# Kernel tuning notes

Measured on AMD Instinct MI355X. Metric: run time of the kernel, lower is better.

## Reference

```python
import jax, jax.numpy as jnp
import numpy as np

B, NS, NQ = 128, 128, 512
D_IN, D_OUT = 256, 64


def setup_inputs() -> dict:
    key = jax.random.key(0)
    ks = jax.random.split(key, 6)
    return {
        "phi_support": jax.random.normal(ks[0], (B, NS, D_IN), dtype=jnp.float32),
        "y_support": jax.random.normal(ks[1], (B, NS, D_OUT), dtype=jnp.float32),
        "phi_query": jax.random.normal(ks[2], (B, NQ, D_IN), dtype=jnp.float32),
        "y_query": jax.random.normal(ks[3], (B, NQ, D_OUT), dtype=jnp.float32),
        # xavier-uniform-ish params
        "m_prior": jax.random.uniform(ks[4], (D_IN, D_OUT), minval=-1.0, maxval=1.0) * np.sqrt(6.0 / (D_IN + D_OUT)),
        "S_inv_prior_asym": jax.random.uniform(ks[5], (D_IN, D_IN), minval=-1.0, maxval=1.0) * np.sqrt(6.0 / (2 * D_IN)),
        "sig_eps": jnp.array([0.1], dtype=jnp.float32),
    }


def reference(phi_support, y_support, phi_query, y_query, m_prior, S_inv_prior_asym, sig_eps):
    alpha = 1.0
    d_out = m_prior.shape[1]
    # prior precision (symmetric PSD by construction) and natural-param prior mean
    S_inv_prior = alpha * (S_inv_prior_asym @ S_inv_prior_asym.T)          # [D_in, D_in]
    m_prior_nat = S_inv_prior @ m_prior                                     # [D_in, D_out]
    # posterior precision / covariance per task (nobs > 0 branch)
    S_inv = jnp.einsum('bni,bnj->bij', phi_support, phi_support) + S_inv_prior  # [B, D_in, D_in]
    S = jnp.linalg.inv(S_inv)                                               # batched small inverse
    rhs = jnp.einsum('bni,bnk->bik', phi_support, y_support) + m_prior_nat  # [B, D_in, D_out]
    m = S @ rhs                                                             # [B, D_in, D_out]
    # predictive mean and spread
    mu = phi_query @ m                                                      # [B, Q, D_out]
    spread_fac = 1.0 + jnp.einsum('bqi,bij,bqj->bq', phi_query, S, phi_query)  # [B, Q]
    # sig = spread_fac (x) (eye * sig_eps) : diagonal [B, Q, D_out, D_out]
    diag = jnp.eye(d_out, dtype=mu.dtype) * sig_eps                         # [D_out, D_out]
    sig = spread_fac[..., None, None] * diag
    # nll: logdet of diagonal sig + quadratic form with its inverse (diag -> reciprocal)
    logdet = d_out * (jnp.log(spread_fac) + jnp.log(sig_eps))               # [B, Q]
    resid = y_query - mu
    quadf = jnp.sum(resid * resid, axis=-1) / (spread_fac * sig_eps)        # [B, Q]
    nll = logdet.mean() + quadf.mean()
    return mu, sig, nll
```

## Files before the change

### kernel.cpp

```cpp
#include <hip/hip_runtime.h>
#include <math.h>

#define B_T   128
#define NS    128
#define NQ    512
#define DIN   256
#define DOUT  64

#define MU_SIZE  (B_T*NQ*DOUT)
#define SIG_SIZE (B_T*NQ*DOUT*DOUT)
#define NLL_IDX  (MU_SIZE + SIG_SIZE)

__global__ __launch_bounds__(256) void k_prior_sp(const float* __restrict__ A,
                                                  double* __restrict__ Sp,
                                                  double* __restrict__ NLLACC) {
    __shared__ float Ai[16][260];
    __shared__ float Aj[16][260];
    int bi = blockIdx.x;
    int i0 = (bi >> 4) << 4;
    int j0 = (bi & 15) << 4;
    int tid = threadIdx.x;
    if (bi == 0 && tid == 0) NLLACC[0] = 0.0;
    for (int idx = tid; idx < 16 * 256; idx += 256) {
        int r = idx >> 8, c = idx & 255;
        Ai[r][c] = A[(i0 + r) * 256 + c];
        Aj[r][c] = A[(j0 + r) * 256 + c];
    }
    __syncthreads();
    int r = tid >> 4, c = tid & 15;
    double acc = 0.0;
    for (int k = 0; k < 256; ++k)
        acc += (double)Ai[r][k] * (double)Aj[c][k];
    Sp[(i0 + r) * 256 + (j0 + c)] = acc;
}

__global__ __launch_bounds__(64) void k_prior_mpn(const double* __restrict__ Sp,
                                                  const float* __restrict__ MP,
                                                  double* __restrict__ MPN) {
    int i = blockIdx.x, k = threadIdx.x;
    double acc = 0.0;
    for (int t = 0; t < 256; ++t)
        acc += Sp[i * 256 + t] * (double)MP[t * 64 + k];
    MPN[i * 64 + k] = acc;
}

__global__ __launch_bounds__(256) void k_build_G(const float* __restrict__ PHI,
                                                 const double* __restrict__ Sp,
                                                 double* __restrict__ G) {
    __shared__ float As[128][64];
    __shared__ float Bs[128][64];
    int b = blockIdx.x;
    int by = blockIdx.y;
    int ti = 0;
    while (((ti + 1) * (ti + 2)) / 2 <= by) ti++;
    int tj = by - (ti * (ti + 1)) / 2;
    int i0 = ti * 64, j0 = tj * 64;
    int tid = threadIdx.x;
    const float* Pb = PHI + b * (NS * DIN);
    for (int idx = tid; idx < 128 * 64; idx += 256) {
        int n = idx >> 6, c = idx & 63;
        As[n][c] = Pb[n * 256 + i0 + c];
        Bs[n][c] = Pb[n * 256 + j0 + c];
    }
    __syncthreads();
    int tx = tid & 15, ty = tid >> 4;
    double acc[4][4];
#pragma unroll
    for (int r = 0; r < 4; ++r)
#pragma unroll
        for (int s = 0; s < 4; ++s) acc[r][s] = 0.0;
    for (int n = 0; n < 128; ++n) {
        float a0 = As[n][4 * ty + 0], a1 = As[n][4 * ty + 1];
        float a2 = As[n][4 * ty + 2], a3 = As[n][4 * ty + 3];
        float b0 = Bs[n][4 * tx + 0], b1 = Bs[n][4 * tx + 1];
        float b2 = Bs[n][4 * tx + 2], b3 = Bs[n][4 * tx + 3];
        acc[0][0] += (double)a0 * b0; acc[0][1] += (double)a0 * b1;
        acc[0][2] += (double)a0 * b2; acc[0][3] += (double)a0 * b3;
        acc[1][0] += (double)a1 * b0; acc[1][1] += (double)a1 * b1;
        acc[1][2] += (double)a1 * b2; acc[1][3] += (double)a1 * b3;
        acc[2][0] += (double)a2 * b0; acc[2][1] += (double)a2 * b1;
        acc[2][2] += (double)a2 * b2; acc[2][3] += (double)a2 * b3;
        acc[3][0] += (double)a3 * b0; acc[3][1] += (double)a3 * b1;
        acc[3][2] += (double)a3 * b2; acc[3][3] += (double)a3 * b3;
    }
    double* Gb = G + b * 65536;
#pragma unroll
    for (int r = 0; r < 4; ++r) {
        int i = i0 + 4 * ty + r;
#pragma unroll
        for (int s = 0; s < 4; ++s) {
            int j = j0 + 4 * tx + s;
            Gb[i * 256 + j] = acc[r][s] + Sp[i * 256 + j];
        }
    }
}

__global__ __launch_bounds__(256) void k_build_rhs(const float* __restrict__ PHI,
                                                   const float* __restrict__ Y,
                                                   const double* __restrict__ MPN,
                                                   double* __restrict__ RHS) {
    __shared__ float As[128][64];
    __shared__ float Ys[128][64];
    int b = blockIdx.x, i0 = blockIdx.y * 64, tid = threadIdx.x;
    const float* Pb = PHI + b * (NS * DIN);
    const float* Yb = Y + b * (NS * DOUT);
    for (int idx = tid; idx < 128 * 64; idx += 256) {
        int n = idx >> 6, c = idx & 63;
        As[n][c] = Pb[n * 256 + i0 + c];
        Ys[n][c] = Yb[n * 64 + c];
    }
    __syncthreads();
    int tx = tid & 15, ty = tid >> 4;
    double acc[4][4];
#pragma unroll
    for (int r = 0; r < 4; ++r)
#pragma unroll
        for (int s = 0; s < 4; ++s) acc[r][s] = 0.0;
    for (int n = 0; n < 128; ++n) {
        float a0 = As[n][4 * ty + 0], a1 = As[n][4 * ty + 1];
        float a2 = As[n][4 * ty + 2], a3 = As[n][4 * ty + 3];
        float y0 = Ys[n][4 * tx + 0], y1 = Ys[n][4 * tx + 1];
        float y2 = Ys[n][4 * tx + 2], y3 = Ys[n][4 * tx + 3];
        acc[0][0] += (double)a0 * y0; acc[0][1] += (double)a0 * y1;
        acc[0][2] += (double)a0 * y2; acc[0][3] += (double)a0 * y3;
        acc[1][0] += (double)a1 * y0; acc[1][1] += (double)a1 * y1;
        acc[1][2] += (double)a1 * y2; acc[1][3] += (double)a1 * y3;
        acc[2][0] += (double)a2 * y0; acc[2][1] += (double)a2 * y1;
        acc[2][2] += (double)a2 * y2; acc[2][3] += (double)a2 * y3;
        acc[3][0] += (double)a3 * y0; acc[3][1] += (double)a3 * y1;
        acc[3][2] += (double)a3 * y2; acc[3][3] += (double)a3 * y3;
    }
    double* Rb = RHS + b * 16384;
#pragma unroll
    for (int r = 0; r < 4; ++r) {
        int i = i0 + 4 * ty + r;
#pragma unroll
        for (int s = 0; s < 4; ++s) {
            int kc = 4 * tx + s;
            Rb[i * 64 + kc] = acc[r][s] + MPN[i * 64 + kc];
        }
    }
}

__global__ __launch_bounds__(256) void k_potrf64(const double* __restrict__ G,
                                                 double* __restrict__ LT,
                                                 double* __restrict__ LI,
                                                 int kb) {
    __shared__ double D[64][65];
    __shared__ double T[64][33];
    __shared__ double C[32][33];
    __shared__ double L11s[16 * 17];
    __shared__ double DINVs[16];
    int b = blockIdx.x, tid = threadIdx.x;
    int o = kb * 64;
    const double* Gb = G + b * 65536;
    double* LTb = LT + b * 65536;
    double* LIb = LI + b * 16384 + kb * 4096;
    for (int idx = tid; idx < 4096; idx += 256) {
        int r = idx >> 6, c = idx & 63;
        D[r][c] = Gb[(o + r) * 256 + o + c];
    }
    __syncthreads();
    for (int p0 = 0; p0 < 64; p0 += 16) {
        if (tid < 64) {
            int lane = tid;
            double a[16];
            if (lane < 16) {
#pragma unroll
                for (int p = 0; p < 16; ++p) a[p] = D[p0 + lane][p0 + p];
            }
#pragma unroll
            for (int p = 0; p < 16; ++p) {
                double dp = __shfl(a[p], p);
                double d = sqrt(fmax(dp, 1e-300));
                double inv = 1.0 / d;
                if (lane == p) { a[p] = d; DINVs[p] = inv; }
                else if (lane > p) a[p] *= inv;
#pragma unroll
                for (int p2 = p + 1; p2 < 16; ++p2) {
                    double cc = __shfl(a[p], p2);
                    if (lane > p) a[p2] -= a[p] * cc;
                }
            }
            if (lane < 16) {
#pragma unroll
                for (int p = 0; p < 16; ++p) {
                    if (p <= lane) {
                        L11s[lane * 17 + p] = a[p];
                        D[p0 + lane][p0 + p] = a[p];
                    }
                }
            }
        }
        __syncthreads();
        int nsolve = 48 - p0;
        if (tid < nsolve) {
            int rr = p0 + 16 + tid;
            double x[16];
#pragma unroll
            for (int p = 0; p < 16; ++p) {
                double s = D[rr][p0 + p];
#pragma unroll
                for (int p2 = 0; p2 < 16; ++p2) {
                    if (p2 < p) s -= L11s[p * 17 + p2] * x[p2];
                }
                x[p] = s * DINVs[p];
                D[rr][p0 + p] = x[p];
            }
        }
        __syncthreads();
        int rem = nsolve;
        for (int idx = tid; idx < rem * rem; idx += 256) {
            int i2 = idx / rem, j2 = idx - i2 * rem;
            if (j2 <= i2) {
                int i = p0 + 16 + i2, j = p0 + 16 + j2;
                double s = 0.0;
#pragma unroll
                for (int p = 0; p < 16; ++p) s += D[i][p0 + p] * D[j][p0 + p];
                D[i][j] -= s;
            }
        }
        __syncthreads();
    }
    for (int idx = tid; idx < 4096; idx += 256) {
        int c = idx >> 6, r = idx & 63;
        if (r >= c) LTb[(o + c) * 256 + (o + r)] = D[r][c];
    }
    if (tid < 64) {
        int g = tid >> 5, j = tid & 31;
        int off = g * 32;
        double x[32];
#pragma unroll
        for (int i = 0; i < 32; ++i) {
            double s = (i == j) ? 1.0 : 0.0;
#pragma unroll
            for (int k = 0; k < i; ++k) {
                double lv = D[off + i][off + k];
                s -= (k >= j) ? lv * x[k] : 0.0;
            }
            double inv = 1.0 / D[off + i][off + i];
            x[i] = (i >= j) ? s * inv : 0.0;
        }
#pragma unroll
        for (int i = 0; i < 32; ++i) T[off + i][j] = x[i];
    }
    __syncthreads();
    for (int idx = tid; idx < 1024; idx += 256) {
        int r = idx >> 5, c = idx & 31;
        double s = 0.0;
#pragma unroll
        for (int p = 0; p < 32; ++p) s += D[32 + r][p] * T[p][c];
        C[r][c] = s;
    }
    __syncthreads();
    for (int idx = tid; idx < 1024; idx += 256) {
        int r = idx >> 5, c = idx & 31;
        double s = 0.0;
#pragma unroll
        for (int p = 0; p < 32; ++p) s += T[32 + r][p] * C[p][c];
        D[32 + r][c] = -s;
    }
    __syncthreads();
    for (int idx = tid; idx < 4096; idx += 256) {
        int p = idx >> 6, c = idx & 63;
        double v;
        if (c < 32) v = (p < 32) ? T[c][p] : 0.0;
        else        v = (p < 32) ? D[c][p] : T[c][p - 32];
        LIb[p * 64 + c] = v;
    }
}

__global__ __launch_bounds__(256) void k_trsm64(const double* __restrict__ G,
                                                const double* __restrict__ LI,
                                                double* __restrict__ LT,
                                                int kb) {
    __shared__ double Gs[64][65];
    __shared__ double Ls[64][65];
    int b = blockIdx.x;
    int i0 = (kb + 1 + blockIdx.y) * 64;
    int o = kb * 64;
    int tid = threadIdx.x;
    const double* Gb = G + b * 65536;
    const double* LIb = LI + b * 16384 + kb * 4096;
    double* LTb = LT + b * 65536;
    for (int idx = tid; idx < 4096; idx += 256) {
        int r = idx >> 6, c = idx & 63;
        Gs[r][c] = Gb[(i0 + r) * 256 + o + c];
        Ls[r][c] = LIb[idx];
    }
    __syncthreads();
    int tx = tid & 15, ty = tid >> 4;
    double acc[4][4];
#pragma unroll
    for (int r = 0; r < 4; ++r)
#pragma unroll
        for (int s = 0; s < 4; ++s) acc[r][s] = 0.0;
    for (int kk = 0; kk < 64; ++kk) {
        double a0 = Gs[4 * ty + 0][kk], a1 = Gs[4 * ty + 1][kk];
        double a2 = Gs[4 * ty + 2][kk], a3 = Gs[4 * ty + 3][kk];
        double b0 = Ls[kk][4 * tx + 0], b1 = Ls[kk][4 * tx + 1];
        double b2 = Ls[kk][4 * tx + 2], b3 = Ls[kk][4 * tx + 3];
        acc[0][0] += a0 * b0; acc[0][1] += a0 * b1; acc[0][2] += a0 * b2; acc[0][3] += a0 * b3;
        acc[1][0] += a1 * b0; acc[1][1] += a1 * b1; acc[1][2] += a1 * b2; acc[1][3] += a1 * b3;
        acc[2][0] += a2 * b0; acc[2][1] += a2 * b1; acc[2][2] += a2 * b2; acc[2][3] += a2 * b3;
        acc[3][0] += a3 * b0; acc[3][1] += a3 * b1; acc[3][2] += a3 * b2; acc[3][3] += a3 * b3;
    }
#pragma unroll
    for (int r = 0; r < 4; ++r)
#pragma unroll
        for (int s = 0; s < 4; ++s)
            LTb[(o + 4 * tx + s) * 256 + i0 + 4 * ty + r] = acc[r][s];
}

__global__ __launch_bounds__(256) void k_syrk64(const double* __restrict__ LT,
                                                double* __restrict__ G,
                                                int kb) {
    __shared__ double LiT[64][65];
    __shared__ double LjT[64][65];
    int b = blockIdx.x, py = blockIdx.y;
    int ti = 0;
    while (((ti + 1) * (ti + 2)) / 2 <= py) ti++;
    int tj = py - (ti * (ti + 1)) / 2;
    int i0 = (kb + 1 + ti) * 64, j0 = (kb + 1 + tj) * 64;
    int o = kb * 64;
    int tid = threadIdx.x;
    const double* LTb = LT + b * 65536;
    double* Gb = G + b * 65536;
    for (int idx = tid; idx < 4096; idx += 256) {
        int p = idx >> 6, r = idx & 63;
        LiT[p][r] = LTb[(o + p) * 256 + i0 + r];
        LjT[p][r] = LTb[(o + p) * 256 + j0 + r];
    }
    __syncthreads();
    int tx = tid & 15, ty = tid >> 4;
    double acc[4][4];
#pragma unroll
    for (int r = 0; r < 4; ++r)
#pragma unroll
        for (int s = 0; s < 4; ++s) acc[r][s] = 0.0;
    for (int kk = 0; kk < 64; ++kk) {
        double a0 = LiT[kk][4 * ty + 0], a1 = LiT[kk][4 * ty + 1];
        double a2 = LiT[kk][4 * ty + 2], a3 = LiT[kk][4 * ty + 3];
        double b0 = LjT[kk][4 * tx + 0], b1 = LjT[kk][4 * tx + 1];
        double b2 = LjT[kk][4 * tx + 2], b3 = LjT[kk][4 * tx + 3];
        acc[0][0] += a0 * b0; acc[0][1] += a0 * b1; acc[0][2] += a0 * b2; acc[0][3] += a0 * b3;
        acc[1][0] += a1 * b0; acc[1][1] += a1 * b1; acc[1][2] += a1 * b2; acc[1][3] += a1 * b3;
        acc[2][0] += a2 * b0; acc[2][1] += a2 * b1; acc[2][2] += a2 * b2; acc[2][3] += a2 * b3;
        acc[3][0] += a3 * b0; acc[3][1] += a3 * b1; acc[3][2] += a3 * b2; acc[3][3] += a3 * b3;
    }
#pragma unroll
    for (int r = 0; r < 4; ++r) {
        int gi = i0 + 4 * ty + r;
#pragma unroll
        for (int s = 0; s < 4; ++s) {
            int gj = j0 + 4 * tx + s;
            Gb[gi * 256 + gj] -= acc[r][s];
        }
    }
}

__global__ __launch_bounds__(256) void k_diaginv(const double* __restrict__ LT,
                                                 double* __restrict__ TI,
                                                 float* __restrict__ TIF) {
    __shared__ double SHD[8192];
    int b = blockIdx.x, tid = threadIdx.x;
    const double* LTb = LT + b * 65536;
    double* TIb = TI + b * 65536;
    float* TIFb = TIF + b * 65536;
    for (int idx = tid; idx < 65536; idx += 256) {
        int i = idx >> 8, k = idx & 255;
        if (k > i) { TIb[idx] = 0.0; TIFb[idx] = 0.0f; }
    }
    for (int idx = tid; idx < 8192; idx += 256) {
        int g = idx >> 10, rem = idx & 1023, k = rem >> 5, i = rem & 31;
        SHD[idx] = LTb[(32 * g + k) * 256 + 32 * g + i];
    }
    __syncthreads();
    int g = tid >> 5, j = tid & 31;
    const double* D = SHD + g * 1024;
    double x[32];
#pragma unroll
    for (int i = 0; i < 32; ++i) {
        double s = (i == j) ? 1.0 : 0.0;
#pragma unroll
        for (int k = 0; k < i; ++k) {
            double lv = D[k * 32 + i];
            s -= (k >= j) ? lv * x[k] : 0.0;
        }
        double inv = 1.0 / D[i * 32 + i];
        x[i] = (i >= j) ? s * inv : 0.0;
    }
#pragma unroll
    for (int i = 0; i < 32; ++i) {
        int gi = 32 * g + i, gj = 32 * g + j;
        TIb[gi * 256 + gj] = x[i];
        TIFb[gi * 256 + gj] = (float)x[i];
    }
}

__global__ __launch_bounds__(256) void k_trinv(const double* __restrict__ LT,
                                               double* __restrict__ TI,
                                               float* __restrict__ TIF) {
    __shared__ double XS[8][1024];
    int b = blockIdx.x, J = blockIdx.y;
    int tid = threadIdx.x, j = tid & 31, ig = tid >> 5;
    const double* LTb = LT + b * 65536;
    double* TIb = TI + b * 65536;
    float* TIFb = TIF + b * 65536;
    double* Bsh = XS[7];

    for (int idx = tid; idx < 1024; idx += 256) {
        int kk = idx >> 5, c = idx & 31;
        XS[J][idx] = TIb[(32 * J + kk) * 256 + 32 * J + c];
    }
    __syncthreads();

    for (int I = J + 1; I < 8; ++I) {
        double acc[4] = {0.0, 0.0, 0.0, 0.0};
        for (int K = J; K < I; ++K) {
            for (int idx = tid; idx < 1024; idx += 256) {
                int kk = idx >> 5, i2 = idx & 31;
                Bsh[idx] = LTb[(32 * K + kk) * 256 + 32 * I + i2];
            }
            __syncthreads();
            const double* Xk = XS[K];
            for (int kk = 0; kk < 32; ++kk) {
                double tv = Xk[kk * 32 + j];
#pragma unroll
                for (int r = 0; r < 4; ++r)
                    acc[r] += Bsh[kk * 32 + ig * 4 + r] * tv;
            }
            __syncthreads();
        }
#pragma unroll
        for (int r = 0; r < 4; ++r) Bsh[(ig * 4 + r) * 32 + j] = acc[r];
        __syncthreads();
        double c[4] = {0.0, 0.0, 0.0, 0.0};
        for (int k = 0; k < 32; ++k) {
            double bv = Bsh[k * 32 + j];
#pragma unroll
            for (int r = 0; r < 4; ++r)
                c[r] -= TIb[(32 * I + ig * 4 + r) * 256 + 32 * I + k] * bv;
        }
#pragma unroll
        for (int r = 0; r < 4; ++r) {
            int gi = 32 * I + ig * 4 + r, gj = 32 * J + j;
            TIb[gi * 256 + gj] = c[r];
            TIFb[gi * 256 + gj] = (float)c[r];
            if (I < 7) XS[I][(ig * 4 + r) * 32 + j] = c[r];
        }
        __syncthreads();
    }
}

__global__ __launch_bounds__(256) void k_gemm_Z(const double* __restrict__ TI,
                                                const double* __restrict__ RHS,
                                                double* __restrict__ Z) {
    __shared__ double As[32][64];
    __shared__ double Bs[64][64];
    int b = blockIdx.x, i0 = blockIdx.y * 32;
    int tid = threadIdx.x, c = tid & 63, rg = tid >> 6;
    const double* TIb = TI + b * 65536;
    const double* Rb = RHS + b * 16384;
    double* Zb = Z + b * 16384;
    double acc[8] = {};
    for (int k0 = 0; k0 <= i0; k0 += 64) {
        for (int idx = tid; idx < 2048; idx += 256) {
            int r = idx >> 6, kk = idx & 63;
            As[r][kk] = TIb[(i0 + r) * 256 + k0 + kk];
        }
        for (int idx = tid; idx < 4096; idx += 256) {
            int kk = idx >> 6, cc = idx & 63;
            Bs[kk][cc] = Rb[(k0 + kk) * 64 + cc];
        }
        __syncthreads();
        for (int kk = 0; kk < 64; ++kk) {
            double bv = Bs[kk][c];
#pragma unroll
            for (int r = 0; r < 8; ++r)
                acc[r] += As[rg * 8 + r][kk] * bv;
        }
        __syncthreads();
    }
#pragma unroll
    for (int r = 0; r < 8; ++r)
        Zb[(i0 + rg * 8 + r) * 64 + c] = acc[r];
}

__global__ __launch_bounds__(256) void k_gemm_M(const double* __restrict__ TI,
                                                const double* __restrict__ Z,
                                                double* __restrict__ M) {
    __shared__ double As[64][32];
    __shared__ double Bs[64][64];
    int b = blockIdx.x, i0 = blockIdx.y * 32;
    int tid = threadIdx.x, c = tid & 63, rg = tid >> 6;
    const double* TIb = TI + b * 65536;
    const double* Zb = Z + b * 16384;
    double* Mb = M + b * 16384;
    double acc[8] = {};
    for (int k0 = (i0 >> 6) << 6; k0 < 256; k0 += 64) {
        for (int idx = tid; idx < 2048; idx += 256) {
            int kk = idx >> 5, ri = idx & 31;
            As[kk][ri] = TIb[(k0 + kk) * 256 + i0 + ri];
        }
        for (int idx = tid; idx < 4096; idx += 256) {
            int kk = idx >> 6, cc = idx & 63;
            Bs[kk][cc] = Zb[(k0 + kk) * 64 + cc];
        }
        __syncthreads();
        for (int kk = 0; kk < 64; ++kk) {
            double bv = Bs[kk][c];
#pragma unroll
            for (int r = 0; r < 8; ++r)
                acc[r] += As[kk][rg * 8 + r] * bv;
        }
        __syncthreads();
    }
#pragma unroll
    for (int r = 0; r < 8; ++r)
        Mb[(i0 + rg * 8 + r) * 64 + c] = acc[r];
}

__global__ __launch_bounds__(256) void k_spread_gemm(const float* __restrict__ PHIQ,
                                                     const float* __restrict__ TIF,
                                                     float* __restrict__ PSUM) {
    __shared__ float Qs[64][65];
    __shared__ float Ts[64][65];
    int b = blockIdx.x, q0 = blockIdx.y * 64, I = blockIdx.z, i0 = I * 64;
    int tid = threadIdx.x, tx = tid & 15, ty = tid >> 4;
    const float* Qb = PHIQ + b * (NQ * DIN) + q0 * DIN;
    const float* Tb = TIF + b * 65536;
    float acc[4][4];
#pragma unroll
    for (int r = 0; r < 4; ++r)
#pragma unroll
        for (int s = 0; s < 4; ++s) acc[r][s] = 0.0f;
    for (int k0 = 0; k0 <= i0; k0 += 64) {
        for (int idx = tid; idx < 4096; idx += 256) {
            int r = idx >> 6, c = idx & 63;
            Qs[r][c] = Qb[r * 256 + k0 + c];
            Ts[c][r] = Tb[(i0 + r) * 256 + k0 + c];
        }
        __syncthreads();
        for (int kk = 0; kk < 64; ++kk) {
            float a0 = Qs[4 * ty + 0][kk], a1 = Qs[4 * ty + 1][kk];
            float a2 = Qs[4 * ty + 2][kk], a3 = Qs[4 * ty + 3][kk];
            float b0 = Ts[kk][4 * tx + 0], b1 = Ts[kk][4 * tx + 1];
            float b2 = Ts[kk][4 * tx + 2], b3 = Ts[kk][4 * tx + 3];
            acc[0][0] += a0 * b0; acc[0][1] += a0 * b1; acc[0][2] += a0 * b2; acc[0][3] += a0 * b3;
            acc[1][0] += a1 * b0; acc[1][1] += a1 * b1; acc[1][2] += a1 * b2; acc[1][3] += a1 * b3;
            acc[2][0] += a2 * b0; acc[2][1] += a2 * b1; acc[2][2] += a2 * b2; acc[2][3] += a2 * b3;
            acc[3][0] += a3 * b0; acc[3][1] += a3 * b1; acc[3][2] += a3 * b2; acc[3][3] += a3 * b3;
        }
        __syncthreads();
    }
#pragma unroll
    for (int r = 0; r < 4; ++r) {
        float p = acc[r][0] * acc[r][0] + acc[r][1] * acc[r][1]
                + acc[r][2] * acc[r][2] + acc[r][3] * acc[r][3];
        p += __shfl_down(p, 8, 16);
        p += __shfl_down(p, 4, 16);
        p += __shfl_down(p, 2, 16);
        p += __shfl_down(p, 1, 16);
        if (tx == 0) PSUM[(size_t)(b * 4 + I) * 512 + q0 + 4 * ty + r] = p;
    }
}

__global__ __launch_bounds__(256) void k_mu_nll(const float* __restrict__ PHIQ,
                                                const double* __restrict__ M,
                                                const float* __restrict__ YQ,
                                                const float* __restrict__ PSUM,
                                                const float* __restrict__ SE,
                                                float* __restrict__ SPREAD,
                                                double* __restrict__ NLLACC,
                                                float* __restrict__ MU) {
    __shared__ float Qs[64][65];
    __shared__ float Ms[64][64];
    __shared__ double nred[64];
    int b = blockIdx.x, q0 = blockIdx.y * 64, tid = threadIdx.x;
    int tx = tid & 15, ty = tid >> 4;
    const float* Qb = PHIQ + b * (NQ * DIN) + q0 * DIN;
    const double* Mb = M + b * 16384;
    float acc[4][4];
#pragma unroll
    for (int r = 0; r < 4; ++r)
#pragma unroll
        for (int s = 0; s < 4; ++s) acc[r][s] = 0.0f;
    for (int c0 = 0; c0 < 256; c0 += 64) {
        for (int idx = tid; idx < 4096; idx += 256) {
            int r = idx >> 6, c = idx & 63;
            Qs[r][c] = Qb[r * 256 + c0 + c];
            Ms[r][c] = (float)Mb[(c0 + r) * 64 + c];
        }
        __syncthreads();
        for (int kk = 0; kk < 64; ++kk) {
            float a0 = Qs[4 * ty + 0][kk], a1 = Qs[4 * ty + 1][kk];
            float a2 = Qs[4 * ty + 2][kk], a3 = Qs[4 * ty + 3][kk];
            float b0 = Ms[kk][4 * tx + 0], b1 = Ms[kk][4 * tx + 1];
            float b2 = Ms[kk][4 * tx + 2], b3 = Ms[kk][4 * tx + 3];
            acc[0][0] += a0 * b0; acc[0][1] += a0 * b1; acc[0][2] += a0 * b2; acc[0][3] += a0 * b3;
            acc[1][0] += a1 * b0; acc[1][1] += a1 * b1; acc[1][2] += a1 * b2; acc[1][3] += a1 * b3;
            acc[2][0] += a2 * b0; acc[2][1] += a2 * b1; acc[2][2] += a2 * b2; acc[2][3] += a2 * b3;
            acc[3][0] += a3 * b0; acc[3][1] += a3 * b1; acc[3][2] += a3 * b2; acc[3][3] += a3 * b3;
        }
        __syncthreads();
    }
    float se = SE[0];
#pragma unroll
    for (int r = 0; r < 4; ++r) {
        int q = q0 + 4 * ty + r;
        float4 v = make_float4(acc[r][0], acc[r][1], acc[r][2], acc[r][3]);
        *(float4*)&MU[(b * NQ + q) * 64 + 4 * tx] = v;
        float4 y = *(const float4*)&YQ[(size_t)(b * NQ + q) * 64 + 4 * tx];
        float dx = y.x - v.x, dy = y.y - v.y, dz = y.z - v.z, dw = y.w - v.w;
        float qs = dx * dx + dy * dy + dz * dz + dw * dw;
        qs += __shfl_down(qs, 8, 16);
        qs += __shfl_down(qs, 4, 16);
        qs += __shfl_down(qs, 2, 16);
        qs += __shfl_down(qs, 1, 16);
        if (tx == 0) {
            float sp = 1.0f + PSUM[(size_t)(b * 4 + 0) * 512 + q]
                            + PSUM[(size_t)(b * 4 + 1) * 512 + q]
                            + PSUM[(size_t)(b * 4 + 2) * 512 + q]
                            + PSUM[(size_t)(b * 4 + 3) * 512 + q];
            SPREAD[b * 512 + q] = sp;
            float val = 64.0f * (logf(sp) + logf(se)) + qs / (sp * se);
            nred[ty * 4 + r] = (double)val;
        }
    }
    __syncthreads();
    for (int s = 32; s > 0; s >>= 1) {
        if (tid < s) nred[tid] += nred[tid + s];
        __syncthreads();
    }
    if (tid == 0) atomicAdd(NLLACC, nred[0] * (1.0 / 65536.0));
}

__global__ void k_nll_final(const double* __restrict__ NLLACC,
                            float* __restrict__ out) {
    if (threadIdx.x == 0) out[NLL_IDX] = (float)NLLACC[0];
}

__global__ __launch_bounds__(256) void k_sig(const float* __restrict__ SPREAD,
                                             const float* __restrict__ SE,
                                             float* __restrict__ out) {
    __shared__ float sv_s;
    int bq = blockIdx.x, tid = threadIdx.x;
    if (tid == 0) sv_s = SPREAD[bq] * SE[0];
    __syncthreads();
    float sv = sv_s;
    float* base = out + (size_t)MU_SIZE + (size_t)bq * 4096;
    int i = tid >> 2;
    int jb = (tid & 3) << 4;
    int d = i - jb;
    float vals[16];
#pragma unroll
    for (int t = 0; t < 16; ++t) vals[t] = (t == d) ? sv : 0.0f;
    float4* p = (float4*)(base + tid * 16);
    p[0] = make_float4(vals[0], vals[1], vals[2], vals[3]);
    p[1] = make_float4(vals[4], vals[5], vals[6], vals[7]);
    p[2] = make_float4(vals[8], vals[9], vals[10], vals[11]);
    p[3] = make_float4(vals[12], vals[13], vals[14], vals[15]);
}

extern "C" void kernel_launch(void* const* d_in, const int* in_sizes, int n_in,
                              void* d_out, int out_size, void* d_ws, size_t ws_size,
                              hipStream_t stream) {
    const float* PHI_S = (const float*)d_in[0];
    const float* Y_S   = (const float*)d_in[1];
    const float* PHI_Q = (const float*)d_in[2];
    const float* Y_Q   = (const float*)d_in[3];
    const float* MP    = (const float*)d_in[4];
    const float* AP    = (const float*)d_in[5];
    const float* SE    = (const float*)d_in[6];
    float* out = (float*)d_out;

    double* scratch = (double*)(out + MU_SIZE);
    double* G    = scratch;
    double* LT   = G + 8388608;
    double* RHS  = LT + 8388608;
    double* Z    = RHS + 2097152;
    double* TI   = Z + 2097152;
    double* Spd  = TI + 8388608;
    double* MPN  = Spd + 65536;
    double* LI   = MPN + 16384;
    float*  TIF  = (float*)(LI + 2097152);
    float*  PSUM = TIF + 8388608;
    float*  SPREAD = (float*)d_ws;
    double* NLLACC = (double*)((char*)d_ws + 65536 * 4);

    k_prior_sp   <<<256, 256, 0, stream>>>(AP, Spd, NLLACC);
    k_prior_mpn  <<<256, 64, 0, stream>>>(Spd, MP, MPN);
    k_build_G    <<<dim3(B_T, 10), 256, 0, stream>>>(PHI_S, Spd, G);
    k_build_rhs  <<<dim3(B_T, 4), 256, 0, stream>>>(PHI_S, Y_S, MPN, RHS);
    const int syrk_pairs[3] = {6, 3, 1};
    for (int kb = 0; kb < 4; ++kb) {
        k_potrf64<<<B_T, 256, 0, stream>>>(G, LT, LI, kb);
        if (kb < 3) {
            k_trsm64<<<dim3(B_T, 3 - kb), 256, 0, stream>>>(G, LI, LT, kb);
            k_syrk64<<<dim3(B_T, syrk_pairs[kb]), 256, 0, stream>>>(LT, G, kb);
        }
    }
    k_diaginv    <<<B_T, 256, 0, stream>>>(LT, TI, TIF);
    k_trinv      <<<dim3(B_T, 7), 256, 0, stream>>>(LT, TI, TIF);
    k_gemm_Z     <<<dim3(B_T, 8), 256, 0, stream>>>(TI, RHS, Z);
    k_gemm_M     <<<dim3(B_T, 8), 256, 0, stream>>>(TI, Z, RHS);
    k_spread_gemm<<<dim3(B_T, 8, 4), 256, 0, stream>>>(PHI_Q, TIF, PSUM);
    k_mu_nll     <<<dim3(B_T, 8), 256, 0, stream>>>(PHI_Q, RHS, Y_Q, PSUM, SE,
                                                    SPREAD, NLLACC, out);
    k_nll_final  <<<1, 64, 0, stream>>>(NLLACC, out);
    k_sig        <<<65536, 256, 0, stream>>>(SPREAD, SE, out);
}
```

Before: 2.090 ms.

## Use FP64 MFMA for small batched GEMMs with runtime layout probe

Replaces the scalar FP64 FMA inner loops in build_G, build_rhs, trsm, syrk and the Z/M GEMMs with 16x16x4 FP64 MFMA intrinsics. A one-wave probe kernel runs first, works out the MFMA output lane-to-element mapping, and writes a flag that each kernel reads to choose its store indexing, falling back to the scalar path if no mapping matches. The Z/M GEMMs also move to 64-row tiles, halving their grids. This targets the FP64 compute-bound parts of the Cholesky-based solve, but adds an extra launch, a flag load per block, and branch code. The total is likely dominated by the large sig output write, which is unchanged.

```diff
diff --git a/kernel.cpp b/kernel.cpp
--- a/kernel.cpp
+++ b/kernel.cpp
@@ -10,6 +10,53 @@
 #define MU_SIZE  (B_T*NQ*DOUT)
 #define SIG_SIZE (B_T*NQ*DOUT*DOUT)
 #define NLL_IDX  (MU_SIZE + SIG_SIZE)
+
+typedef double v4df __attribute__((ext_vector_type(4)));
+
+__device__ __forceinline__ void dmap(int fl, int kq, int mrow, int rr,
+                                     int& lr, int& lc) {
+    if (fl == 0)      { lr = kq * 4 + rr; lc = mrow; }
+    else if (fl == 1) { lr = kq + 4 * rr; lc = mrow; }
+    else if (fl == 2) { lr = mrow; lc = kq * 4 + rr; }
+    else              { lr = mrow; lc = kq + 4 * rr; }
+}
+
+__global__ void k_mfma_probe(double* __restrict__ FLAGD) {
+    int l = threadIdx.x;
+    int m = l & 15, q = l >> 4;
+    double a = (double)(1 + m + 2 * q);
+    double b = (double)(1 + 3 * m + 5 * q);
+    v4df d = {0.0, 0.0, 0.0, 0.0};
+    d = __builtin_amdgcn_mfma_f64_16x16x4f64(a, b, d, 0, 0, 0);
+    bool ok0 = true, ok1 = true, ok2 = true, ok3 = true;
+#pragma unroll
+    for (int r = 0; r < 4; ++r) {
+        int rows[4] = {4 * q + r, q + 4 * r, m, m};
+        int cols[4] = {m, m, 4 * q + r, q + 4 * r};
+        double ref[4];
+#pragma unroll
+        for (int v = 0; v < 4; ++v) {
+            double s = 0.0;
+#pragma unroll
+            for (int k = 0; k < 4; ++k)
+                s += (double)(1 + rows[v] + 2 * k) * (double)(1 + 3 * cols[v] + 5 * k);
+            ref[v] = s;
+        }
+        if (d[r] != ref[0]) ok0 = false;
+        if (d[r] != ref[1]) ok1 = false;
+        if (d[r] != ref[2]) ok2 = false;
+        if (d[r] != ref[3]) ok3 = false;
+    }
+    ok0 = __all(ok0); ok1 = __all(ok1); ok2 = __all(ok2); ok3 = __all(ok3);
+    if (l == 0) {
+        double f = 99.0;
+        if (ok0) f = 0.0;
+        else if (ok1) f = 1.0;
+        else if (ok2) f = 2.0;
+        else if (ok3) f = 3.0;
+        FLAGD[0] = f;
+    }
+}
 
 __global__ __launch_bounds__(256) void k_prior_sp(const float* __restrict__ A,
                                                   double* __restrict__ Sp,
@@ -46,7 +93,8 @@
 
 __global__ __launch_bounds__(256) void k_build_G(const float* __restrict__ PHI,
                                                  const double* __restrict__ Sp,
-                                                 double* __restrict__ G) {
+                                                 double* __restrict__ G,
+                                                 const double* __restrict__ FLAGD) {
     __shared__ float As[128][64];
     __shared__ float Bs[128][64];
     int b = blockIdx.x;
@@ -63,34 +111,61 @@
         Bs[n][c] = Pb[n * 256 + j0 + c];
     }
     __syncthreads();
-    int tx = tid & 15, ty = tid >> 4;
-    double acc[4][4];
-#pragma unroll
-    for (int r = 0; r < 4; ++r)
-#pragma unroll
-        for (int s = 0; s < 4; ++s) acc[r][s] = 0.0;
-    for (int n = 0; n < 128; ++n) {
-        float a0 = As[n][4 * ty + 0], a1 = As[n][4 * ty + 1];
-        float a2 = As[n][4 * ty + 2], a3 = As[n][4 * ty + 3];
-        float b0 = Bs[n][4 * tx + 0], b1 = Bs[n][4 * tx + 1];
-        float b2 = Bs[n][4 * tx + 2], b3 = Bs[n][4 * tx + 3];
-        acc[0][0] += (double)a0 * b0; acc[0][1] += (double)a0 * b1;
-        acc[0][2] += (double)a0 * b2; acc[0][3] += (double)a0 * b3;
-        acc[1][0] += (double)a1 * b0; acc[1][1] += (double)a1 * b1;
-        acc[1][2] += (double)a1 * b2; acc[1][3] += (double)a1 * b3;
-        acc[2][0] += (double)a2 * b0; acc[2][1] += (double)a2 * b1;
-        acc[2][2] += (double)a2 * b2; acc[2][3] += (double)a2 * b3;
-        acc[3][0] += (double)a3 * b0; acc[3][1] += (double)a3 * b1;
-        acc[3][2] += (double)a3 * b2; acc[3][3] += (double)a3 * b3;
-    }
     double* Gb = G + b * 65536;
-#pragma unroll
-    for (int r = 0; r < 4; ++r) {
-        int i = i0 + 4 * ty + r;
-#pragma unroll
-        for (int s = 0; s < 4; ++s) {
-            int j = j0 + 4 * tx + s;
-            Gb[i * 256 + j] = acc[r][s] + Sp[i * 256 + j];
+    int fl = (int)FLAGD[0];
+    if (fl < 4) {
+        int lane = tid & 63, w = tid >> 6;
+        int mrow = lane & 15, kq = lane >> 4;
+        v4df acc[4];
+#pragma unroll
+        for (int t = 0; t < 4; ++t) acc[t] = (v4df){0.0, 0.0, 0.0, 0.0};
+        for (int ks = 0; ks < 128; ks += 4) {
+            double a = (double)As[ks + kq][w * 16 + mrow];
+#pragma unroll
+            for (int t = 0; t < 4; ++t) {
+                double bb = (double)Bs[ks + kq][t * 16 + mrow];
+                acc[t] = __builtin_amdgcn_mfma_f64_16x16x4f64(a, bb, acc[t], 0, 0, 0);
+            }
+        }
+#pragma unroll
+        for (int t = 0; t < 4; ++t) {
+#pragma unroll
+            for (int rr = 0; rr < 4; ++rr) {
+                int lr, lc; dmap(fl, kq, mrow, rr, lr, lc);
+                int i = i0 + w * 16 + lr;
+                int j = j0 + t * 16 + lc;
+                Gb[i * 256 + j] = acc[t][rr] + Sp[i * 256 + j];
+            }
+        }
+    } else {
+        int tx = tid & 15, ty = tid >> 4;
+        double acc[4][4];
+#pragma unroll
+        for (int r = 0; r < 4; ++r)
+#pragma unroll
+            for (int s = 0; s < 4; ++s) acc[r][s] = 0.0;
+        for (int n = 0; n < 128; ++n) {
+            float a0 = As[n][4 * ty + 0], a1 = As[n][4 * ty + 1];
+            float a2 = As[n][4 * ty + 2], a3 = As[n][4 * ty + 3];
+            float b0 = Bs[n][4 * tx + 0], b1 = Bs[n][4 * tx + 1];
+            float b2 = Bs[n][4 * tx + 2], b3 = Bs[n][4 * tx + 3];
+            acc[0][0] += (double)a0 * b0; acc[0][1] += (double)a0 * b1;
+            acc[0][2] += (double)a0 * b2; acc[0][3] += (double)a0 * b3;
+            acc[1][0] += (double)a1 * b0; acc[1][1] += (double)a1 * b1;
+            acc[1][2] += (double)a1 * b2; acc[1][3] += (double)a1 * b3;
+            acc[2][0] += (double)a2 * b0; acc[2][1] += (double)a2 * b1;
+            acc[2][2] += (double)a2 * b2; acc[2][3] += (double)a2 * b3;
+            acc[3][0] += (double)a3 * b0; acc[3][1] += (double)a3 * b1;
+            acc[3][2] += (double)a3 * b2; acc[3][3] += (double)a3 * b3;
+        }
+#pragma unroll
+        for (int r = 0; r < 4; ++r) {
+            int i = i0 + 4 * ty + r;
+#pragma unroll
+            for (int s = 0; s < 4; ++s) {
+                int j = j0 + 4 * tx + s;
+                Gb[i * 256 + j] = acc[r][s] + Sp[i * 256 + j];
+            }
         }
     }
 }
@@ -98,7 +173,8 @@
 __global__ __launch_bounds__(256) void k_build_rhs(const float* __restrict__ PHI,
                                                    const float* __restrict__ Y,
                                                    const double* __restrict__ MPN,
-                                                   double* __restrict__ RHS) {
+                                                   double* __restrict__ RHS,
+                                                   const double* __restrict__ FLAGD) {
     __shared__ float As[128][64];
     __shared__ float Ys[128][64];
     int b = blockIdx.x, i0 = blockIdx.y * 64, tid = threadIdx.x;
@@ -110,34 +186,61 @@
         Ys[n][c] = Yb[n * 64 + c];
     }
     __syncthreads();
-    int tx = tid & 15, ty = tid >> 4;
-    double acc[4][4];
-#pragma unroll
-    for (int r = 0; r < 4; ++r)
-#pragma unroll
-        for (int s = 0; s < 4; ++s) acc[r][s] = 0.0;
-    for (int n = 0; n < 128; ++n) {
-        float a0 = As[n][4 * ty + 0], a1 = As[n][4 * ty + 1];
-        float a2 = As[n][4 * ty + 2], a3 = As[n][4 * ty + 3];
-        float y0 = Ys[n][4 * tx + 0], y1 = Ys[n][4 * tx + 1];
-        float y2 = Ys[n][4 * tx + 2], y3 = Ys[n][4 * tx + 3];
-        acc[0][0] += (double)a0 * y0; acc[0][1] += (double)a0 * y1;
-        acc[0][2] += (double)a0 * y2; acc[0][3] += (double)a0 * y3;
-        acc[1][0] += (double)a1 * y0; acc[1][1] += (double)a1 * y1;
-        acc[1][2] += (double)a1 * y2; acc[1][3] += (double)a1 * y3;
-        acc[2][0] += (double)a2 * y0; acc[2][1] += (double)a2 * y1;
-        acc[2][2] += (double)a2 * y2; acc[2][3] += (double)a2 * y3;
-        acc[3][0] += (double)a3 * y0; acc[3][1] += (double)a3 * y1;
-        acc[3][2] += (double)a3 * y2; acc[3][3] += (double)a3 * y3;
-    }
     double* Rb = RHS + b * 16384;
-#pragma unroll
-    for (int r = 0; r < 4; ++r) {
-        int i = i0 + 4 * ty + r;
-#pragma unroll
-        for (int s = 0; s < 4; ++s) {
-            int kc = 4 * tx + s;
-            Rb[i * 64 + kc] = acc[r][s] + MPN[i * 64 + kc];
+    int fl = (int)FLAGD[0];
+    if (fl < 4) {
+        int lane = tid & 63, w = tid >> 6;
+        int mrow = lane & 15, kq = lane >> 4;
+        v4df acc[4];
+#pragma unroll
+        for (int t = 0; t < 4; ++t) acc[t] = (v4df){0.0, 0.0, 0.0, 0.0};
+        for (int ks = 0; ks < 128; ks += 4) {
+            double a = (double)As[ks + kq][w * 16 + mrow];
+#pragma unroll
+            for (int t = 0; t < 4; ++t) {
+                double bb = (double)Ys[ks + kq][t * 16 + mrow];
+                acc[t] = __builtin_amdgcn_mfma_f64_16x16x4f64(a, bb, acc[t], 0, 0, 0);
+            }
+        }
+#pragma unroll
+        for (int t = 0; t < 4; ++t) {
+#pragma unroll
+            for (int rr = 0; rr < 4; ++rr) {
+                int lr, lc; dmap(fl, kq, mrow, rr, lr, lc);
+                int i = i0 + w * 16 + lr;
+                int kc = t * 16 + lc;
+                Rb[i * 64 + kc] = acc[t][rr] + MPN[i * 64 + kc];
+            }
+        }
+    } else {
+        int tx = tid & 15, ty = tid >> 4;
+        double acc[4][4];
+#pragma unroll
+        for (int r = 0; r < 4; ++r)
+#pragma unroll
+            for (int s = 0; s < 4; ++s) acc[r][s] = 0.0;
+        for (int n = 0; n < 128; ++n) {
+            float a0 = As[n][4 * ty + 0], a1 = As[n][4 * ty + 1];
+            float a2 = As[n][4 * ty + 2], a3 = As[n][4 * ty + 3];
+            float y0 = Ys[n][4 * tx + 0], y1 = Ys[n][4 * tx + 1];
+            float y2 = Ys[n][4 * tx + 2], y3 = Ys[n][4 * tx + 3];
+            acc[0][0] += (double)a0 * y0; acc[0][1] += (double)a0 * y1;
+            acc[0][2] += (double)a0 * y2; acc[0][3] += (double)a0 * y3;
+            acc[1][0] += (double)a1 * y0; acc[1][1] += (double)a1 * y1;
+            acc[1][2] += (double)a1 * y2; acc[1][3] += (double)a1 * y3;
+            acc[2][0] += (double)a2 * y0; acc[2][1] += (double)a2 * y1;
+            acc[2][2] += (double)a2 * y2; acc[2][3] += (double)a2 * y3;
+            acc[3][0] += (double)a3 * y0; acc[3][1] += (double)a3 * y1;
+            acc[3][2] += (double)a3 * y2; acc[3][3] += (double)a3 * y3;
+        }
+#pragma unroll
+        for (int r = 0; r < 4; ++r) {
+            int i = i0 + 4 * ty + r;
+#pragma unroll
+            for (int s = 0; s < 4; ++s) {
+                int kc = 4 * tx + s;
+                Rb[i * 64 + kc] = acc[r][s] + MPN[i * 64 + kc];
+            }
         }
     }
 }
@@ -273,7 +376,8 @@
 __global__ __launch_bounds__(256) void k_trsm64(const double* __restrict__ G,
                                                 const double* __restrict__ LI,
                                                 double* __restrict__ LT,
-                                                int kb) {
+                                                int kb,
+                                                const double* __restrict__ FLAGD) {
     __shared__ double Gs[64][65];
     __shared__ double Ls[64][65];
     int b = blockIdx.x;
@@ -289,32 +393,60 @@
         Ls[r][c] = LIb[idx];
     }
     __syncthreads();
-    int tx = tid & 15, ty = tid >> 4;
-    double acc[4][4];
-#pragma unroll
-    for (int r = 0; r < 4; ++r)
-#pragma unroll
-        for (int s = 0; s < 4; ++s) acc[r][s] = 0.0;
-    for (int kk = 0; kk < 64; ++kk) {
-        double a0 = Gs[4 * ty + 0][kk], a1 = Gs[4 * ty + 1][kk];
-        double a2 = Gs[4 * ty + 2][kk], a3 = Gs[4 * ty + 3][kk];
-        double b0 = Ls[kk][4 * tx + 0], b1 = Ls[kk][4 * tx + 1];
-        double b2 = Ls[kk][4 * tx + 2], b3 = Ls[kk][4 * tx + 3];
-        acc[0][0] += a0 * b0; acc[0][1] += a0 * b1; acc[0][2] += a0 * b2; acc[0][3] += a0 * b3;
-        acc[1][0] += a1 * b0; acc[1][1] += a1 * b1; acc[1][2] += a1 * b2; acc[1][3] += a1 * b3;
-        acc[2][0] += a2 * b0; acc[2][1] += a2 * b1; acc[2][2] += a2 * b2; acc[2][3] += a2 * b3;
-        acc[3][0] += a3 * b0; acc[3][1] += a3 * b1; acc[3][2] += a3 * b2; acc[3][3] += a3 * b3;
-    }
-#pragma unroll
-    for (int r = 0; r < 4; ++r)
-#pragma unroll
-        for (int s = 0; s < 4; ++s)
-            LTb[(o + 4 * tx + s) * 256 + i0 + 4 * ty + r] = acc[r][s];
+    int fl = (int)FLAGD[0];
+    if (fl < 4) {
+        int lane = tid & 63, w = tid >> 6;
+        int mrow = lane & 15, kq = lane >> 4;
+        v4df acc[4];
+#pragma unroll
+        for (int t = 0; t < 4; ++t) acc[t] = (v4df){0.0, 0.0, 0.0, 0.0};
+        for (int ks = 0; ks < 64; ks += 4) {
+            double a = Gs[w * 16 + mrow][ks + kq];
+#pragma unroll
+            for (int t = 0; t < 4; ++t) {
+                double bb = Ls[ks + kq][t * 16 + mrow];
+                acc[t] = __builtin_amdgcn_mfma_f64_16x16x4f64(a, bb, acc[t], 0, 0, 0);
+            }
+        }
+#pragma unroll
+        for (int t = 0; t < 4; ++t) {
+#pragma unroll
+            for (int rr = 0; rr < 4; ++rr) {
+                int lr, lc; dmap(fl, kq, mrow, rr, lr, lc);
+                int r = w * 16 + lr;
+                int c = t * 16 + lc;
+                LTb[(o + c) * 256 + i0 + r] = acc[t][rr];
+            }
+        }
+    } else {
+        int tx = tid & 15, ty = tid >> 4;
+        double acc[4][4];
+#pragma unroll
+        for (int r = 0; r < 4; ++r)
+#pragma unroll
+            for (int s = 0; s < 4; ++s) acc[r][s] = 0.0;
+        for (int kk = 0; kk < 64; ++kk) {
+            double a0 = Gs[4 * ty + 0][kk], a1 = Gs[4 * ty + 1][kk];
+            double a2 = Gs[4 * ty + 2][kk], a3 = Gs[4 * ty + 3][kk];
+            double b0 = Ls[kk][4 * tx + 0], b1 = Ls[kk][4 * tx + 1];
+            double b2 = Ls[kk][4 * tx + 2], b3 = Ls[kk][4 * tx + 3];
+            acc[0][0] += a0 * b0; acc[0][1] += a0 * b1; acc[0][2] += a0 * b2; acc[0][3] += a0 * b3;
+            acc[1][0] += a1 * b0; acc[1][1] += a1 * b1; acc[1][2] += a1 * b2; acc[1][3] += a1 * b3;
+            acc[2][0] += a2 * b0; acc[2][1] += a2 * b1; acc[2][2] += a2 * b2; acc[2][3] += a2 * b3;
+            acc[3][0] += a3 * b0; acc[3][1] += a3 * b1; acc[3][2] += a3 * b2; acc[3][3] += a3 * b3;
+        }
+#pragma unroll
+        for (int r = 0; r < 4; ++r)
+#pragma unroll
+            for (int s = 0; s < 4; ++s)
+                LTb[(o + 4 * tx + s) * 256 + i0 + 4 * ty + r] = acc[r][s];
+    }
 }
 
 __global__ __launch_bounds__(256) void k_syrk64(const double* __restrict__ LT,
                                                 double* __restrict__ G,
-                                                int kb) {
+                                                int kb,
+                                                const double* __restrict__ FLAGD) {
     __shared__ double LiT[64][65];
     __shared__ double LjT[64][65];
     int b = blockIdx.x, py = blockIdx.y;
@@ -332,29 +464,56 @@
         LjT[p][r] = LTb[(o + p) * 256 + j0 + r];
     }
     __syncthreads();
-    int tx = tid & 15, ty = tid >> 4;
-    double acc[4][4];
-#pragma unroll
-    for (int r = 0; r < 4; ++r)
-#pragma unroll
-        for (int s = 0; s < 4; ++s) acc[r][s] = 0.0;
-    for (int kk = 0; kk < 64; ++kk) {
-        double a0 = LiT[kk][4 * ty + 0], a1 = LiT[kk][4 * ty + 1];
-        double a2 = LiT[kk][4 * ty + 2], a3 = LiT[kk][4 * ty + 3];
-        double b0 = LjT[kk][4 * tx + 0], b1 = LjT[kk][4 * tx + 1];
-        double b2 = LjT[kk][4 * tx + 2], b3 = LjT[kk][4 * tx + 3];
-        acc[0][0] += a0 * b0; acc[0][1] += a0 * b1; acc[0][2] += a0 * b2; acc[0][3] += a0 * b3;
-        acc[1][0] += a1 * b0; acc[1][1] += a1 * b1; acc[1][2] += a1 * b2; acc[1][3] += a1 * b3;
-        acc[2][0] += a2 * b0; acc[2][1] += a2 * b1; acc[2][2] += a2 * b2; acc[2][3] += a2 * b3;
-        acc[3][0] += a3 * b0; acc[3][1] += a3 * b1; acc[3][2] += a3 * b2; acc[3][3] += a3 * b3;
-    }
-#pragma unroll
-    for (int r = 0; r < 4; ++r) {
-        int gi = i0 + 4 * ty + r;
-#pragma unroll
-        for (int s = 0; s < 4; ++s) {
-            int gj = j0 + 4 * tx + s;
-            Gb[gi * 256 + gj] -= acc[r][s];
+    int fl = (int)FLAGD[0];
+    if (fl < 4) {
+        int lane = tid & 63, w = tid >> 6;
+        int mrow = lane & 15, kq = lane >> 4;
+        v4df acc[4];
+#pragma unroll
+        for (int t = 0; t < 4; ++t) acc[t] = (v4df){0.0, 0.0, 0.0, 0.0};
+        for (int ks = 0; ks < 64; ks += 4) {
+            double a = LiT[ks + kq][w * 16 + mrow];
+#pragma unroll
+            for (int t = 0; t < 4; ++t) {
+                double bb = LjT[ks + kq][t * 16 + mrow];
+                acc[t] = __builtin_amdgcn_mfma_f64_16x16x4f64(a, bb, acc[t], 0, 0, 0);
+            }
+        }
+#pragma unroll
+        for (int t = 0; t < 4; ++t) {
+#pragma unroll
+            for (int rr = 0; rr < 4; ++rr) {
+                int lr, lc; dmap(fl, kq, mrow, rr, lr, lc);
+                int gi = i0 + w * 16 + lr;
+                int gj = j0 + t * 16 + lc;
+                Gb[gi * 256 + gj] -= acc[t][rr];
+            }
+        }
+    } else {
+        int tx = tid & 15, ty = tid >> 4;
+        double acc[4][4];
+#pragma unroll
+        for (int r = 0; r < 4; ++r)
+#pragma unroll
+            for (int s = 0; s < 4; ++s) acc[r][s] = 0.0;
+        for (int kk = 0; kk < 64; ++kk) {
+            double a0 = LiT[kk][4 * ty + 0], a1 = LiT[kk][4 * ty + 1];
+            double a2 = LiT[kk][4 * ty + 2], a3 = LiT[kk][4 * ty + 3];
+            double b0 = LjT[kk][4 * tx + 0], b1 = LjT[kk][4 * tx + 1];
+            double b2 = LjT[kk][4 * tx + 2], b3 = LjT[kk][4 * tx + 3];
+            acc[0][0] += a0 * b0; acc[0][1] += a0 * b1; acc[0][2] += a0 * b2; acc[0][3] += a0 * b3;
+            acc[1][0] += a1 * b0; acc[1][1] += a1 * b1; acc[1][2] += a1 * b2; acc[1][3] += a1 * b3;
+            acc[2][0] += a2 * b0; acc[2][1] += a2 * b1; acc[2][2] += a2 * b2; acc[2][3] += a2 * b3;
+            acc[3][0] += a3 * b0; acc[3][1] += a3 * b1; acc[3][2] += a3 * b2; acc[3][3] += a3 * b3;
+        }
+#pragma unroll
+        for (int r = 0; r < 4; ++r) {
+            int gi = i0 + 4 * ty + r;
+#pragma unroll
+            for (int s = 0; s < 4; ++s) {
+                int gj = j0 + 4 * tx + s;
+                Gb[gi * 256 + gj] -= acc[r][s];
+            }
         }
     }
 }
@@ -455,70 +614,140 @@
 
 __global__ __launch_bounds__(256) void k_gemm_Z(const double* __restrict__ TI,
                                                 const double* __restrict__ RHS,
-                                                double* __restrict__ Z) {
-    __shared__ double As[32][64];
-    __shared__ double Bs[64][64];
-    int b = blockIdx.x, i0 = blockIdx.y * 32;
-    int tid = threadIdx.x, c = tid & 63, rg = tid >> 6;
+                                                double* __restrict__ Z,
+                                                const double* __restrict__ FLAGD) {
+    __shared__ double As[64][65];
+    __shared__ double Bs[64][65];
+    int b = blockIdx.x, i0 = blockIdx.y * 64;
+    int tid = threadIdx.x;
     const double* TIb = TI + b * 65536;
     const double* Rb = RHS + b * 16384;
     double* Zb = Z + b * 16384;
-    double acc[8] = {};
-    for (int k0 = 0; k0 <= i0; k0 += 64) {
-        for (int idx = tid; idx < 2048; idx += 256) {
-            int r = idx >> 6, kk = idx & 63;
-            As[r][kk] = TIb[(i0 + r) * 256 + k0 + kk];
-        }
-        for (int idx = tid; idx < 4096; idx += 256) {
-            int kk = idx >> 6, cc = idx & 63;
-            Bs[kk][cc] = Rb[(k0 + kk) * 64 + cc];
-        }
-        __syncthreads();
-        for (int kk = 0; kk < 64; ++kk) {
-            double bv = Bs[kk][c];
-#pragma unroll
-            for (int r = 0; r < 8; ++r)
-                acc[r] += As[rg * 8 + r][kk] * bv;
-        }
-        __syncthreads();
-    }
-#pragma unroll
-    for (int r = 0; r < 8; ++r)
-        Zb[(i0 + rg * 8 + r) * 64 + c] = acc[r];
+    int fl = (int)FLAGD[0];
+    if (fl < 4) {
+        int lane = tid & 63, w = tid >> 6;
+        int mrow = lane & 15, kq = lane >> 4;
+        v4df acc[4];
+#pragma unroll
+        for (int t = 0; t < 4; ++t) acc[t] = (v4df){0.0, 0.0, 0.0, 0.0};
+        for (int k0 = 0; k0 <= i0; k0 += 64) {
+            for (int idx = tid; idx < 4096; idx += 256) {
+                int r = idx >> 6, kk = idx & 63;
+                As[r][kk] = TIb[(i0 + r) * 256 + k0 + kk];
+                Bs[r][kk] = Rb[(k0 + r) * 64 + kk];
+            }
+            __syncthreads();
+            for (int ks = 0; ks < 64; ks += 4) {
+                double a = As[w * 16 + mrow][ks + kq];
+#pragma unroll
+                for (int t = 0; t < 4; ++t) {
+                    double bb = Bs[ks + kq][t * 16 + mrow];
+                    acc[t] = __builtin_amdgcn_mfma_f64_16x16x4f64(a, bb, acc[t], 0, 0, 0);
+                }
+            }
+            __syncthreads();
+        }
+#pragma unroll
+        for (int t = 0; t < 4; ++t) {
+#pragma unroll
+            for (int rr = 0; rr < 4; ++rr) {
+                int lr, lc; dmap(fl, kq, mrow, rr, lr, lc);
+                Zb[(i0 + w * 16 + lr) * 64 + t * 16 + lc] = acc[t][rr];
+            }
+        }
+    } else {
+        int c = tid & 63, rg = tid >> 6;
+        double acc[16];
+#pragma unroll
+        for (int r = 0; r < 16; ++r) acc[r] = 0.0;
+        for (int k0 = 0; k0 <= i0; k0 += 64) {
+            for (int idx = tid; idx < 4096; idx += 256) {
+                int r = idx >> 6, kk = idx & 63;
+                As[r][kk] = TIb[(i0 + r) * 256 + k0 + kk];
+                Bs[r][kk] = Rb[(k0 + r) * 64 + kk];
+            }
+            __syncthreads();
+            for (int kk = 0; kk < 64; ++kk) {
+                double bv = Bs[kk][c];
+#pragma unroll
+                for (int r = 0; r < 16; ++r)
+                    acc[r] += As[rg * 16 + r][kk] * bv;
+            }
+            __syncthreads();
+        }
+#pragma unroll
+        for (int r = 0; r < 16; ++r)
+            Zb[(i0 + rg * 16 + r) * 64 + c] = acc[r];
+    }
 }
 
 __global__ __launch_bounds__(256) void k_gemm_M(const double* __restrict__ TI,
                                                 const double* __restrict__ Z,
-                                                double* __restrict__ M) {
-    __shared__ double As[64][32];
-    __shared__ double Bs[64][64];
-    int b = blockIdx.x, i0 = blockIdx.y * 32;
-    int tid = threadIdx.x, c = tid & 63, rg = tid >> 6;
+                                                double* __restrict__ M,
+                                                const double* __restrict__ FLAGD) {
+    __shared__ double As[64][65];
+    __shared__ double Bs[64][65];
+    int b = blockIdx.x, i0 = blockIdx.y * 64;
+    int tid = threadIdx.x;
     const double* TIb = TI + b * 65536;
     const double* Zb = Z + b * 16384;
     double* Mb = M + b * 16384;
-    double acc[8] = {};
-    for (int k0 = (i0 >> 6) << 6; k0 < 256; k0 += 64) {
-        for (int idx = tid; idx < 2048; idx += 256) {
-            int kk = idx >> 5, ri = idx & 31;
-            As[kk][ri] = TIb[(k0 + kk) * 256 + i0 + ri];
-        }
-        for (int idx = tid; idx < 4096; idx += 256) {
-            int kk = idx >> 6, cc = idx & 63;
-            Bs[kk][cc] = Zb[(k0 + kk) * 64 + cc];
-        }
-        __syncthreads();
-        for (int kk = 0; kk < 64; ++kk) {
-            double bv = Bs[kk][c];
-#pragma unroll
-            for (int r = 0; r < 8; ++r)
-                acc[r] += As[kk][rg * 8 + r] * bv;
-        }
-        __syncthreads();
-    }
-#pragma unroll
-    for (int r = 0; r < 8; ++r)
-        Mb[(i0 + rg * 8 + r) * 64 + c] = acc[r];
+    int fl = (int)FLAGD[0];
+    if (fl < 4) {
+        int lane = tid & 63, w = tid >> 6;
+        int mrow = lane & 15, kq = lane >> 4;
+        v4df acc[4];
+#pragma unroll
+        for (int t = 0; t < 4; ++t) acc[t] = (v4df){0.0, 0.0, 0.0, 0.0};
+        for (int k0 = i0; k0 < 256; k0 += 64) {
+            for (int idx = tid; idx < 4096; idx += 256) {
+                int kk = idx >> 6, m = idx & 63;
+                As[kk][m] = TIb[(k0 + kk) * 256 + i0 + m];
+                Bs[kk][m] = Zb[(k0 + kk) * 64 + m];
+            }
+            __syncthreads();
+            for (int ks = 0; ks < 64; ks += 4) {
+                double a = As[ks + kq][w * 16 + mrow];
+#pragma unroll
+                for (int t = 0; t < 4; ++t) {
+                    double bb = Bs[ks + kq][t * 16 + mrow];
+                    acc[t] = __builtin_amdgcn_mfma_f64_16x16x4f64(a, bb, acc[t], 0, 0, 0);
+                }
+            }
+            __syncthreads();
+        }
+#pragma unroll
+        for (int t = 0; t < 4; ++t) {
+#pragma unroll
+            for (int rr = 0; rr < 4; ++rr) {
+                int lr, lc; dmap(fl, kq, mrow, rr, lr, lc);
+                Mb[(i0 + w * 16 + lr) * 64 + t * 16 + lc] = acc[t][rr];
+            }
+        }
+    } else {
+        int c = tid & 63, rg = tid >> 6;
+        double acc[16];
+#pragma unroll
+        for (int r = 0; r < 16; ++r) acc[r] = 0.0;
+        for (int k0 = i0; k0 < 256; k0 += 64) {
+            for (int idx = tid; idx < 4096; idx += 256) {
+                int kk = idx >> 6, m = idx & 63;
+                As[kk][m] = TIb[(k0 + kk) * 256 + i0 + m];
+                Bs[kk][m] = Zb[(k0 + kk) * 64 + m];
+            }
+            __syncthreads();
+            for (int kk = 0; kk < 64; ++kk) {
+                double bv = Bs[kk][c];
+#pragma unroll
+                for (int r = 0; r < 16; ++r)
+                    acc[r] += As[kk][rg * 16 + r] * bv;
+            }
+            __syncthreads();
+        }
+#pragma unroll
+        for (int r = 0; r < 16; ++r)
+            Mb[(i0 + rg * 16 + r) * 64 + c] = acc[r];
+    }
 }
 
 __global__ __launch_bounds__(256) void k_spread_gemm(const float* __restrict__ PHIQ,
@@ -688,23 +917,25 @@
     float*  PSUM = TIF + 8388608;
     float*  SPREAD = (float*)d_ws;
     double* NLLACC = (double*)((char*)d_ws + 65536 * 4);
-
+    double* FLAGD  = (double*)((char*)d_ws + 65536 * 4 + 8);
+
+    k_mfma_probe <<<1, 64, 0, stream>>>(FLAGD);
     k_prior_sp   <<<256, 256, 0, stream>>>(AP, Spd, NLLACC);
     k_prior_mpn  <<<256, 64, 0, stream>>>(Spd, MP, MPN);
-    k_build_G    <<<dim3(B_T, 10), 256, 0, stream>>>(PHI_S, Spd, G);
-    k_build_rhs  <<<dim3(B_T, 4), 256, 0, stream>>>(PHI_S, Y_S, MPN, RHS);
+    k_build_G    <<<dim3(B_T, 10), 256, 0, stream>>>(PHI_S, Spd, G, FLAGD);
+    k_build_rhs  <<<dim3(B_T, 4), 256, 0, stream>>>(PHI_S, Y_S, MPN, RHS, FLAGD);
     const int syrk_pairs[3] = {6, 3, 1};
     for (int kb = 0; kb < 4; ++kb) {
         k_potrf64<<<B_T, 256, 0, stream>>>(G, LT, LI, kb);
         if (kb < 3) {
-            k_trsm64<<<dim3(B_T, 3 - kb), 256, 0, stream>>>(G, LI, LT, kb);
-            k_syrk64<<<dim3(B_T, syrk_pairs[kb]), 256, 0, stream>>>(LT, G, kb);
+            k_trsm64<<<dim3(B_T, 3 - kb), 256, 0, stream>>>(G, LI, LT, kb, FLAGD);
+            k_syrk64<<<dim3(B_T, syrk_pairs[kb]), 256, 0, stream>>>(LT, G, kb, FLAGD);
         }
     }
     k_diaginv    <<<B_T, 256, 0, stream>>>(LT, TI, TIF);
     k_trinv      <<<dim3(B_T, 7), 256, 0, stream>>>(LT, TI, TIF);
-    k_gemm_Z     <<<dim3(B_T, 8), 256, 0, stream>>>(TI, RHS, Z);
-    k_gemm_M     <<<dim3(B_T, 8), 256, 0, stream>>>(TI, Z, RHS);
+    k_gemm_Z     <<<dim3(B_T, 4), 256, 0, stream>>>(TI, RHS, Z, FLAGD);
+    k_gemm_M     <<<dim3(B_T, 4), 256, 0, stream>>>(TI, Z, RHS, FLAGD);
     k_spread_gemm<<<dim3(B_T, 8, 4), 256, 0, stream>>>(PHI_Q, TIF, PSUM);
     k_mu_nll     <<<dim3(B_T, 8), 256, 0, stream>>>(PHI_Q, RHS, Y_Q, PSUM, SE,
                                                     SPREAD, NLLACC, out);
```

Measured after the change: 2.074 ms. About the same (-0.7%).
